# Kernel optimization log

Measured on AMD Instinct MI355X. Metric: run time of the kernel, lower is better.

Reference implementation:

```python
import jax, jax.numpy as jnp
import numpy as np


def setup_inputs() -> dict:
    key = jax.random.key(0)
    inp = jax.random.normal(key, (8, 3, 224, 224), dtype=jnp.float32)
    return {"inp": inp, "tau_min": 1, "tau_max": 60, "ntau": 8,
            "num_angles": 12, "stride": 2}


def _logpolar_offsets(tau_min, tau_max, ntau, num_angles):
    # Matches the torch module: theta in [-pi, pi), tau logarithmically spaced,
    # coords stacked angle-major as (y, x) pairs (theta unsqueeze(1) outer).
    c = (tau_max / tau_min) ** (1.0 / (ntau - 1)) - 1.0
    theta = np.arange(num_angles, dtype=np.float64) * (2.0 * np.pi / num_angles) - np.pi
    tau = tau_min * (1.0 + c) ** np.arange(ntau, dtype=np.float64)
    x = tau[None, :] * np.cos(theta[:, None])   # (A, T)
    y = tau[None, :] * np.sin(theta[:, None])   # (A, T)
    return (jnp.asarray(y.ravel(), jnp.float32),
            jnp.asarray(x.ravel(), jnp.float32))  # each (A*T,)


def reference(inp, tau_min, tau_max, ntau, num_angles, stride):
    yoff, xoff = _logpolar_offsets(tau_min, tau_max, ntau, num_angles)
    B, F, H, W = inp.shape
    Hs = (H - 1) // stride + 1
    Ws = (W - 1) // stride + 1
    gy = jnp.arange(Hs, dtype=jnp.float32) * stride   # focus-point rows
    gx = jnp.arange(Ws, dtype=jnp.float32) * stride   # focus-point cols

    def sample(yo, xo):
        # Bilinear sample of inp at (i*stride + yo, j*stride + xo), zero outside.
        yq = gy + yo
        xq = gx + xo
        y0 = jnp.floor(yq)
        x0 = jnp.floor(xq)
        wy = (yq - y0)  # (Hs,)
        wx = (xq - x0)  # (Ws,)
        y0i = y0.astype(jnp.int32)
        x0i = x0.astype(jnp.int32)

        def gather(yi, xi):
            vy = ((yi >= 0) & (yi < H)).astype(inp.dtype)
            vx = ((xi >= 0) & (xi < W)).astype(inp.dtype)
            g = inp[:, :, jnp.clip(yi, 0, H - 1), :][:, :, :, jnp.clip(xi, 0, W - 1)]
            return g * (vy[:, None] * vx[None, :])  # (B,F,Hs,Ws)

        w00 = (1 - wy)[:, None] * (1 - wx)[None, :]
        w01 = (1 - wy)[:, None] * wx[None, :]
        w10 = wy[:, None] * (1 - wx)[None, :]
        w11 = wy[:, None] * wx[None, :]
        return (w00 * gather(y0i, x0i) + w01 * gather(y0i, x0i + 1)
                + w10 * gather(y0i + 1, x0i) + w11 * gather(y0i + 1, x0i + 1))

    out = jax.vmap(sample)(yoff, xoff)                    # (A*T, B, F, Hs, Ws)
    out = out.reshape(num_angles, ntau, B, F, Hs, Ws)
    out = jnp.transpose(out, (2, 3, 1, 0, 4, 5))          # (B, F, ntau, A, Hs, Ws)
    return out
```

## Files before the change

### kernel.cpp

```cpp
#include <hip/hip_runtime.h>
#include <cmath>

#ifndef M_PI
#define M_PI 3.14159265358979323846
#endif

#define B_ 8
#define F_ 3
#define H_ 224
#define W_ 224
#define T_ 8
#define A_ 12
#define NK 96
#define STRIDE_ 2
#define HS_ 112
#define WS_ 112
#define PLANE_ (H_ * W_)
#define SLICE_ (HS_ * WS_)

#define RI 4
#define BAND (2 * RI + 119)

struct LPArgs {
    int   cx[NK];
    int   cy[NK];
    float fx[NK];
    float fy[NK];
};

static LPArgs make_args() {
    LPArgs r;
    double c = pow(60.0, 1.0 / 7.0) - 1.0;
    for (int t = 0; t < T_; ++t) {
        double tau = pow(1.0 + c, (double)t);
        for (int ang = 0; ang < A_; ++ang) {
            double theta = (double)ang * (2.0 * M_PI / (double)A_) - M_PI;
            float yo = (float)(tau * sin(theta));
            float xo = (float)(tau * cos(theta));
            int k = t * A_ + ang;
            float yf = floorf(yo), xf = floorf(xo);
            r.cy[k] = (int)yf; r.fy[k] = yo - yf;
            r.cx[k] = (int)xf; r.fx[k] = xo - xf;
        }
    }
    return r;
}

__global__ __launch_bounds__(1024) void lp_sample_kernel(
    const float* __restrict__ inp, float* __restrict__ out, LPArgs args) {

    __shared__ float lds[BAND * W_];

    const int bf  = blockIdx.x;
    const int i0  = blockIdx.y * RI;
    const int r0  = max(0, 2 * i0 - 60);
    const int r1  = min(H_ - 1, 2 * i0 + 2 * RI + 58);
    const int tid = threadIdx.x;

    const float* plane = inp + (size_t)bf * PLANE_;

    {
        const float4* src4 = (const float4*)(plane + r0 * W_);
        float4*       dst4 = (float4*)lds;
        const int n4 = (r1 - r0 + 1) * (W_ / 4);
        for (int v = tid; v < n4; v += 1024) dst4[v] = src4[v];
    }
    __syncthreads();

    const int lane = tid & 63;
    const int wave = __builtin_amdgcn_readfirstlane(tid >> 6);
    const int di   = wave & 3;
    const int kb   = wave >> 2;
    const int i    = i0 + di;

    float* outbase = out + (size_t)bf * NK * SLICE_ + (size_t)i * WS_;

#pragma unroll 1
    for (int n = 0; n < 24; ++n) {
        const int k = kb + 4 * n;
        const int   cy = args.cy[k]; const float fy = args.fy[k];
        const int   cx = args.cx[k]; const float fx = args.fx[k];

        const int iy0 = 2 * i + cy;
        float mA, mB;
        if (iy0 >= 0 && iy0 <= H_ - 2)  { mA = 1.0f - fy; mB = fy; }
        else if (iy0 == -1)             { mA = fy;        mB = 0.0f; }
        else if (iy0 == H_ - 1)         { mA = 0.0f;      mB = 1.0f - fy; }
        else                            { mA = 0.0f;      mB = 0.0f; }
        const int by = min(max(iy0, 0), H_ - 2);
        const float* lrow = lds + (by - r0) * W_;

        float* orow = outbase + (size_t)k * SLICE_;

#pragma unroll
        for (int h = 0; h < 2; ++h) {
            const int j   = h * 64 + lane;
            const int ix0 = 2 * j + cx;
            float wA, wB;
            if (ix0 >= 0 && ix0 <= W_ - 2)  { wA = 1.0f - fx; wB = fx; }
            else if (ix0 == -1)             { wA = fx;        wB = 0.0f; }
            else if (ix0 == W_ - 1)         { wA = 0.0f;      wB = 1.0f - fx; }
            else                            { wA = 0.0f;      wB = 0.0f; }
            const int bx = min(max(ix0, 0), W_ - 2);

            float g00 = lrow[bx],      g01 = lrow[bx + 1];
            float g10 = lrow[W_ + bx], g11 = lrow[W_ + bx + 1];

            float r = mA * (wA * g00 + wB * g01)
                    + mB * (wA * g10 + wB * g11);

            if (h == 0 || j < WS_) orow[j] = r;
        }
    }
}

extern "C" void kernel_launch(void* const* d_in, const int* in_sizes, int n_in,
                              void* d_out, int out_size, void* d_ws, size_t ws_size,
                              hipStream_t stream) {
    const float* inp = (const float*)d_in[0];
    float*       out = (float*)d_out;

    static const LPArgs args = make_args();

    dim3 grid(B_ * F_, HS_ / RI);
    lp_sample_kernel<<<grid, 1024, 0, stream>>>(inp, out, args);
}
```

Measured before the change: 153.0 us.

## Split offsets into two cy-sorted groups to shrink the LDS row band

Offsets are sorted by their integer y shift on the host and split into two groups of 48, each handled by its own block along a new grid z dimension. Each block loads only the input rows its group needs, so the LDS band drops from about 127 rows to at most 70. That shrinks shared memory per block and may let more blocks stay resident. The work per wave is also reorganised so each task covers one offset and one half of a row across all four output rows. This doubles the block count and the plane loads into LDS, and output writes become scattered through a korig permutation.

```diff
diff --git a/kernel.cpp b/kernel.cpp
--- a/kernel.cpp
+++ b/kernel.cpp
@@ -1,5 +1,6 @@
 #include <hip/hip_runtime.h>
 #include <cmath>
+#include <algorithm>
 
 #ifndef M_PI
 #define M_PI 3.14159265358979323846
@@ -19,29 +20,41 @@
 #define SLICE_ (HS_ * WS_)
 
 #define RI 4
-#define BAND (2 * RI + 119)
+#define BANDMAX 70
 
 struct LPArgs {
-    int   cx[NK];
-    int   cy[NK];
-    float fx[NK];
-    float fy[NK];
+    int   cy[NK];  int cx[NK];
+    float fy[NK];  float fx[NK];
+    int   korig[NK];
+    int   cymin[2]; int cymax[2];
 };
 
 static LPArgs make_args() {
-    LPArgs r;
+    int cy[NK], cx[NK]; float fy[NK], fx[NK];
     double c = pow(60.0, 1.0 / 7.0) - 1.0;
     for (int t = 0; t < T_; ++t) {
         double tau = pow(1.0 + c, (double)t);
-        for (int ang = 0; ang < A_; ++ang) {
-            double theta = (double)ang * (2.0 * M_PI / (double)A_) - M_PI;
-            float yo = (float)(tau * sin(theta));
-            float xo = (float)(tau * cos(theta));
-            int k = t * A_ + ang;
+        for (int a = 0; a < A_; ++a) {
+            double th = (double)a * (2.0 * M_PI / (double)A_) - M_PI;
+            float yo = (float)(tau * sin(th)), xo = (float)(tau * cos(th));
+            int k = t * A_ + a;
             float yf = floorf(yo), xf = floorf(xo);
-            r.cy[k] = (int)yf; r.fy[k] = yo - yf;
-            r.cx[k] = (int)xf; r.fx[k] = xo - xf;
+            cy[k] = (int)yf; fy[k] = yo - yf;
+            cx[k] = (int)xf; fx[k] = xo - xf;
         }
+    }
+    int idx[NK];
+    for (int k = 0; k < NK; ++k) idx[k] = k;
+    std::sort(idx, idx + NK, [&](int a, int b) { return cy[a] < cy[b]; });
+    LPArgs r;
+    r.cymin[0] = r.cymin[1] = 1000; r.cymax[0] = r.cymax[1] = -1000;
+    for (int p = 0; p < NK; ++p) {
+        int k = idx[p], g = p / 48;
+        r.cy[p] = cy[k]; r.cx[p] = cx[k];
+        r.fy[p] = fy[k]; r.fx[p] = fx[k];
+        r.korig[p] = k;
+        r.cymin[g] = std::min(r.cymin[g], cy[k]);
+        r.cymax[g] = std::max(r.cymax[g], cy[k]);
     }
     return r;
 }
@@ -49,67 +62,71 @@
 __global__ __launch_bounds__(1024) void lp_sample_kernel(
     const float* __restrict__ inp, float* __restrict__ out, LPArgs args) {
 
-    __shared__ float lds[BAND * W_];
+    __shared__ float lds[BANDMAX * W_];
 
-    const int bf  = blockIdx.x;
-    const int i0  = blockIdx.y * RI;
-    const int r0  = max(0, 2 * i0 - 60);
-    const int r1  = min(H_ - 1, 2 * i0 + 2 * RI + 58);
-    const int tid = threadIdx.x;
+    const int bf = blockIdx.x;
+    const int i0 = blockIdx.y * RI;
+    const int g  = blockIdx.z;
+
+    const int r0 = max(0, 2 * i0 + args.cymin[g]);
+    const int r1 = min(H_ - 1, 2 * i0 + 2 * (RI - 1) + args.cymax[g] + 1);
 
     const float* plane = inp + (size_t)bf * PLANE_;
-
     {
-        const float4* src4 = (const float4*)(plane + r0 * W_);
-        float4*       dst4 = (float4*)lds;
+        const float4* s4 = (const float4*)(plane + r0 * W_);
+        float4*       d4 = (float4*)lds;
         const int n4 = (r1 - r0 + 1) * (W_ / 4);
-        for (int v = tid; v < n4; v += 1024) dst4[v] = src4[v];
+        for (int v = threadIdx.x; v < n4; v += 1024) d4[v] = s4[v];
     }
     __syncthreads();
 
-    const int lane = tid & 63;
-    const int wave = __builtin_amdgcn_readfirstlane(tid >> 6);
-    const int di   = wave & 3;
-    const int kb   = wave >> 2;
-    const int i    = i0 + di;
+    const int lane = threadIdx.x & 63;
+    const int wave = __builtin_amdgcn_readfirstlane(threadIdx.x >> 6);
 
-    float* outbase = out + (size_t)bf * NK * SLICE_ + (size_t)i * WS_;
+    float* outp = out + (size_t)bf * (NK * SLICE_) + (size_t)i0 * WS_;
 
 #pragma unroll 1
-    for (int n = 0; n < 24; ++n) {
-        const int k = kb + 4 * n;
-        const int   cy = args.cy[k]; const float fy = args.fy[k];
-        const int   cx = args.cx[k]; const float fx = args.fx[k];
+    for (int tt = 0; tt < 6; ++tt) {
+        const int task = wave + (tt << 4);
+        const int kl   = task >> 1;
+        const int h    = task & 1;
+        const int kk   = g * 48 + kl;
 
-        const int iy0 = 2 * i + cy;
-        float mA, mB;
-        if (iy0 >= 0 && iy0 <= H_ - 2)  { mA = 1.0f - fy; mB = fy; }
-        else if (iy0 == -1)             { mA = fy;        mB = 0.0f; }
-        else if (iy0 == H_ - 1)         { mA = 0.0f;      mB = 1.0f - fy; }
-        else                            { mA = 0.0f;      mB = 0.0f; }
-        const int by = min(max(iy0, 0), H_ - 2);
-        const float* lrow = lds + (by - r0) * W_;
+        const int   cy = args.cy[kk]; const float fy = args.fy[kk];
+        const int   cx = args.cx[kk]; const float fx = args.fx[kk];
+        const int   ko = args.korig[kk];
 
-        float* orow = outbase + (size_t)k * SLICE_;
+        const int j   = h * 64 + lane;
+        const int ix0 = 2 * j + cx;
+        float wA, wB;
+        if (ix0 >= 0 && ix0 <= W_ - 2)  { wA = 1.0f - fx; wB = fx; }
+        else if (ix0 == -1)             { wA = fx;        wB = 0.0f; }
+        else if (ix0 == W_ - 1)         { wA = 0.0f;      wB = 1.0f - fx; }
+        else                            { wA = 0.0f;      wB = 0.0f; }
+        const int bx = min(max(ix0, 0), W_ - 2);
+        const float* lcol = lds + bx;
+
+        float* orow = outp + (size_t)ko * SLICE_ + j;
+        const bool act = (j < WS_);
 
 #pragma unroll
-        for (int h = 0; h < 2; ++h) {
-            const int j   = h * 64 + lane;
-            const int ix0 = 2 * j + cx;
-            float wA, wB;
-            if (ix0 >= 0 && ix0 <= W_ - 2)  { wA = 1.0f - fx; wB = fx; }
-            else if (ix0 == -1)             { wA = fx;        wB = 0.0f; }
-            else if (ix0 == W_ - 1)         { wA = 0.0f;      wB = 1.0f - fx; }
-            else                            { wA = 0.0f;      wB = 0.0f; }
-            const int bx = min(max(ix0, 0), W_ - 2);
+        for (int di = 0; di < RI; ++di) {
+            const int iy0 = 2 * (i0 + di) + cy;
+            float mA, mB;
+            if (iy0 >= 0 && iy0 <= H_ - 2)  { mA = 1.0f - fy; mB = fy; }
+            else if (iy0 == -1)             { mA = fy;        mB = 0.0f; }
+            else if (iy0 == H_ - 1)         { mA = 0.0f;      mB = 1.0f - fy; }
+            else                            { mA = 0.0f;      mB = 0.0f; }
+            const int by = min(max(iy0, 0), H_ - 2);
 
-            float g00 = lrow[bx],      g01 = lrow[bx + 1];
-            float g10 = lrow[W_ + bx], g11 = lrow[W_ + bx + 1];
+            const float* p = lcol + (by - r0) * W_;
+            float g00 = p[0],   g01 = p[1];
+            float g10 = p[W_],  g11 = p[W_ + 1];
 
             float r = mA * (wA * g00 + wB * g01)
                     + mB * (wA * g10 + wB * g11);
 
-            if (h == 0 || j < WS_) orow[j] = r;
+            if (act) orow[(size_t)di * WS_] = r;
         }
     }
 }
@@ -122,6 +139,6 @@
 
     static const LPArgs args = make_args();
 
-    dim3 grid(B_ * F_, HS_ / RI);
+    dim3 grid(B_ * F_, HS_ / RI, 2);
     lp_sample_kernel<<<grid, 1024, 0, stream>>>(inp, out, args);
 }
```

Result: faster. 134.4 us (-12.2%).
